# Performance work log

Hardware: AMD Instinct MI355X
Metric: run time of the kernel (lower is better)

## Reference

```python
import jax, jax.numpy as jnp
import numpy as np

EPS = 0.001  # epsilon used by both custom layer norms in the source
B, T, D, H, O = 64, 1024, 128, 256, 64


def setup_inputs() -> dict:
    key = jax.random.key(0)
    ks = jax.random.split(key, 8)
    s = 0.05
    return {
        "x": jax.random.normal(ks[0], (B, T, D), jnp.float32),
        "Wi": jax.random.normal(ks[1], (4 * H, D), jnp.float32) * s,   # input_weights
        "bi": jax.random.normal(ks[2], (4 * H,), jnp.float32) * s,
        "Wh": jax.random.normal(ks[3], (4 * H, H), jnp.float32) * s,   # hidden_weights
        "bh": jax.random.normal(ks[4], (4 * H,), jnp.float32) * s,
        "lna_gamma": jnp.ones((4 * H,), jnp.float32),
        "lna_beta": jnp.zeros((4 * H,), jnp.float32),
        "ln_gamma": jnp.ones((H,), jnp.float32),
        "ln_beta": jnp.zeros((H,), jnp.float32),
        "Wf": jax.random.normal(ks[5], (O, H), jnp.float32) * s,       # fc
        "bf": jax.random.normal(ks[6], (O,), jnp.float32) * s,
    }


def _ln(x, gamma, beta):
    # custom layer norm: mean/var over last axis, eps=1e-3 (no Bessel correction)
    m = jnp.mean(x, axis=-1, keepdims=True)
    xs = x - m
    v = jnp.mean(xs * xs, axis=-1, keepdims=True)
    return gamma * (xs / jnp.sqrt(v + EPS)) + beta


def reference(x, Wi, bi, Wh, bh, lna_gamma, lna_beta, ln_gamma, ln_beta, Wf, bf):
    b, t, d = x.shape
    h = Wh.shape[1]
    # precompute input projections for all timesteps: (T, B, 4H)
    xproj = jnp.einsum('btd,gd->tbg', x, Wi) + bi

    def step(carry, xp_t):
        hx, cx = carry                              # (B, H) each
        gates = xp_t + hx @ Wh.T + bh               # (B, 4H)
        # layer_norm_all: normalize each of the 4 gate blocks over H
        g4 = gates.reshape(b, 4, h)
        m = jnp.mean(g4, axis=-1, keepdims=True)
        gs = g4 - m
        v = jnp.mean(gs * gs, axis=-1, keepdims=True)
        gates = (gs / jnp.sqrt(v + EPS)).reshape(b, 4 * h) * lna_gamma + lna_beta
        ig, fg, cg, og = jnp.split(gates, 4, axis=1)
        ig = jax.nn.sigmoid(ig)
        fg = jax.nn.sigmoid(fg)
        cg = jnp.tanh(cg)
        og = jax.nn.sigmoid(og)
        cy = fg * cx + ig * cg
        hy = og * jnp.tanh(_ln(cy, ln_gamma, ln_beta))
        return (hy, cy), hy

    h0 = jnp.zeros((b, h), x.dtype)
    c0 = jnp.zeros((b, h), x.dtype)
    _, hs = jax.lax.scan(step, (h0, c0), xproj)     # hs: (T, B, H)
    out = hs.transpose(1, 0, 2)                     # (B, T, H)
    yhat = jax.nn.relu(out @ Wf.T + bf)             # (B, T, O)
    return yhat
```

## Files before the change

### kernel.cpp

```cpp
#include <hip/hip_runtime.h>

#define T_TOT 1024
#define BB 64
#define DD 128
#define HH 256
#define GG 1024
#define OO 64
#define LN_EPS 1e-3f
#define NBR 45
#define NBL 19

typedef unsigned int u32;
typedef _Float16 h2 __attribute__((ext_vector_type(2)));
typedef _Float16 f16x8 __attribute__((ext_vector_type(8)));
typedef float f32x4 __attribute__((ext_vector_type(4)));

__device__ __forceinline__ float fdot2(u32 a, u32 b, float c) {
  return __builtin_amdgcn_fdot2(__builtin_bit_cast(h2, a), __builtin_bit_cast(h2, b), c, false);
}
__device__ __forceinline__ u32 pkf16(float lo, float hi) {
  h2 v = { (_Float16)lo, (_Float16)hi };
  return __builtin_bit_cast(u32, v);
}
__device__ __forceinline__ float fast_sigmoid(float x) { return 1.0f / (1.0f + __expf(-x)); }
__device__ __forceinline__ float fast_tanh(float x) { return 2.0f / (1.0f + __expf(-2.0f * x)) - 1.0f; }

__global__ void prep_bfrag(const float* __restrict__ Wh, uint4* __restrict__ bfragG) {
  int id = blockIdx.x * 256 + threadIdx.x;
  int lane = id & 63, tile = (id >> 6) & 63, w = id >> 12;
  int t = tile >> 3, n = tile & 7;
  int col = w * 128 + n * 16 + (lane & 15);
  int k0 = t * 32 + (lane >> 4) * 8;
  const float* p = Wh + (size_t)col * HH + k0;
  uint4 o;
  o.x = pkf16(p[0], p[1]); o.y = pkf16(p[2], p[3]);
  o.z = pkf16(p[4], p[5]); o.w = pkf16(p[6], p[7]);
  bfragG[id] = o;
}

__global__ void prep_wi(const float* __restrict__ Wi, uint4* __restrict__ wip4) {
  int id = blockIdx.x * 256 + threadIdx.x;
  int kp4 = id >> 10, g = id & 1023;
  const float* p = Wi + (size_t)g * DD + kp4 * 8;
  uint4 o;
  o.x = pkf16(p[0], p[1]); o.y = pkf16(p[2], p[3]);
  o.z = pkf16(p[4], p[5]); o.w = pkf16(p[6], p[7]);
  wip4[id] = o;
}

__global__ __launch_bounds__(256) void xproj_gemm(
    const float* __restrict__ x, const uint4* __restrict__ wip4,
    const float* __restrict__ bi, const float* __restrict__ bh,
    _Float16* __restrict__ xph, int m0) {
  __shared__ _Float16 xl[16][128];
  const int tid = threadIdx.x;
  const int mt = blockIdx.x, gt = blockIdx.y;
  const int g = gt * 256 + tid;
  const int woff = ((g >> 7) << 7) | ((g & 15) << 3) | ((g >> 4) & 7);
#pragma unroll
  for (int i = 0; i < 8; ++i) {
    int idx = i * 256 + tid;
    int p = idx >> 7, d = idx & 127;
    int m = m0 + mt * 16 + p;
    xl[p][d] = (_Float16)x[(size_t)(m & 63) * (T_TOT * DD) + (size_t)(m >> 6) * DD + d];
  }
  __syncthreads();
  float acc[16];
#pragma unroll
  for (int p = 0; p < 16; ++p) acc[p] = 0.f;
#pragma unroll
  for (int kp4 = 0; kp4 < 16; ++kp4) {
    uint4 w = wip4[kp4 * GG + g];
#pragma unroll
    for (int p = 0; p < 16; ++p) {
      uint4 hv = *(const uint4*)(&xl[p][kp4 * 8]);
      acc[p] = fdot2(w.x, hv.x, acc[p]);
      acc[p] = fdot2(w.y, hv.y, acc[p]);
      acc[p] = fdot2(w.z, hv.z, acc[p]);
      acc[p] = fdot2(w.w, hv.w, acc[p]);
    }
  }
  float bsum = bi[g] + bh[g];
#pragma unroll
  for (int p = 0; p < 16; ++p) {
    int ml = mt * 16 + p;
    xph[(size_t)ml * GG + woff] = (_Float16)(acc[p] + bsum);
  }
}

__global__ __attribute__((amdgpu_flat_work_group_size(512, 512), amdgpu_waves_per_eu(2, 2)))
void lstm_scan(
    const uint4* __restrict__ bfragG, const _Float16* __restrict__ xphf,
    const float* __restrict__ lna_g, const float* __restrict__ lna_b,
    const float* __restrict__ ln_g, const float* __restrict__ ln_b,
    _Float16* __restrict__ hs16,
    _Float16* __restrict__ hxst, float* __restrict__ cxst,
    int t0, int ct) {
  extern __shared__ char smem[];
  f16x8* wl = (f16x8*)smem;
  _Float16* hx16 = (_Float16*)(smem + 155648);
  float* red  = (float*)(smem + 156160);
  float* red2 = (float*)(smem + 156224);
  float* gact = (float*)(smem + 156256);

  const int tid = threadIdx.x, b = blockIdx.x;
  const int lane = tid & 63, wid = tid >> 6, q = wid >> 1;
  const int l4 = lane & 15;

  const uint4* bw = bfragG + wid * 4096;
  f16x8 breg[NBR];
#pragma unroll
  for (int i = 0; i < NBR; ++i) breg[i] = __builtin_bit_cast(f16x8, bw[i * 64 + lane]);
#pragma unroll
  for (int i = NBR; i < 64; ++i)
    wl[(wid * NBL + (i - NBR)) * 64 + lane] = __builtin_bit_cast(f16x8, bw[i * 64 + lane]);

  u32 lgp[4], lbp[4];
#pragma unroll
  for (int k = 0; k < 4; ++k) {
    int g0 = wid * 128 + (2 * k) * 16 + l4;
    lgp[k] = pkf16(lna_g[g0], lna_g[g0 + 16]);
    lbp[k] = pkf16(lna_b[g0], lna_b[g0 + 16]);
  }
  float lng = 0.f, lnb = 0.f, cx = 0.f;
  if (tid < HH) {
    lng = ln_g[tid]; lnb = ln_b[tid];
    if (t0 == 0) {
      hx16[tid] = (_Float16)0.f;
    } else {
      hx16[tid] = hxst[b * HH + tid]; cx = cxst[b * HH + tid];
    }
  }
  __syncthreads();

  const _Float16* xrow = xphf + (size_t)b * GG + wid * 128 + l4 * 8;
  _Float16* hsp = hs16 + (size_t)b * HH + (tid & 255);

  f16x8 xp = *(const f16x8*)xrow;
  for (int tl = 0; tl < ct; ++tl) {
    f32x4 acc[8];
#pragma unroll
    for (int n = 0; n < 8; ++n) acc[n] = (f32x4){0.f, 0.f, 0.f, 0.f};
#pragma unroll
    for (int t = 0; t < 8; ++t) {
      uint4 hv = *(const uint4*)(hx16 + t * 32 + ((lane >> 4) << 3));
      uint4 az;
      az.x = (l4 == 0) ? hv.x : 0u;
      az.y = (l4 == 0) ? hv.y : 0u;
      az.z = (l4 == 0) ? hv.z : 0u;
      az.w = (l4 == 0) ? hv.w : 0u;
      f16x8 afr = __builtin_bit_cast(f16x8, az);
#pragma unroll
      for (int n = 0; n < 8; ++n) {
        const int idx = t * 8 + n;
        f16x8 bfr;
        if (idx < NBR) bfr = breg[idx];
        else           bfr = wl[(wid * NBL + (idx - NBR)) * 64 + lane];
        acc[n] = __builtin_amdgcn_mfma_f32_16x16x32_f16(afr, bfr, acc[n], 0, 0, 0);
      }
    }
    float g8[8];
#pragma unroll
    for (int n = 0; n < 8; ++n) g8[n] = acc[n][0] + (float)xp[n];
    if (tl + 1 < ct) xp = *(const f16x8*)(xrow + (size_t)(tl + 1) * (BB * GG));

    float s = 0.f, ss = 0.f;
#pragma unroll
    for (int n = 0; n < 8; ++n) { s += g8[n]; ss += g8[n] * g8[n]; }
#pragma unroll
    for (int m = 1; m <= 8; m <<= 1) {
      s += __shfl_xor(s, m, 64);
      ss += __shfl_xor(ss, m, 64);
    }
    if (lane == 0) { red[wid] = s; red[8 + wid] = ss; }
    __syncthreads();
    float S  = red[2 * q] + red[2 * q + 1];
    float SS = red[8 + 2 * q] + red[8 + 2 * q + 1];
    float mean = S * (1.f / HH);
    float var = SS * (1.f / HH) - mean * mean;
    float rstd = rsqrtf(var + LN_EPS);
    if (lane < 16) {
#pragma unroll
      for (int n = 0; n < 8; ++n) {
        h2 lgv = __builtin_bit_cast(h2, lgp[n >> 1]);
        h2 lbv = __builtin_bit_cast(h2, lbp[n >> 1]);
        float gn = (g8[n] - mean) * rstd * (float)lgv[n & 1] + (float)lbv[n & 1];
        float av = (q == 2) ? fast_tanh(gn) : fast_sigmoid(gn);
        gact[wid * 128 + n * 16 + lane] = av;
      }
    }
    __syncthreads();

    float cy = 0.f;
    if (tid < HH) {
      int h = tid;
      cy = gact[HH + h] * cx + gact[h] * gact[2 * HH + h];
      cx = cy;
      float s2 = cy, ss2 = cy * cy;
#pragma unroll
      for (int m = 1; m <= 32; m <<= 1) {
        s2 += __shfl_xor(s2, m, 64);
        ss2 += __shfl_xor(ss2, m, 64);
      }
      if (lane == 0) { red2[wid] = s2; red2[4 + wid] = ss2; }
    }
    __syncthreads();
    if (tid < HH) {
      int h = tid;
      float S2  = red2[0] + red2[1] + red2[2] + red2[3];
      float SS2 = red2[4] + red2[5] + red2[6] + red2[7];
      float mc = S2 * (1.f / HH);
      float vc = SS2 * (1.f / HH) - mc * mc;
      float cyn = (cy - mc) * rsqrtf(vc + LN_EPS) * lng + lnb;
      float hy = gact[3 * HH + h] * fast_tanh(cyn);
      hx16[h] = (_Float16)hy;
      hsp[(size_t)(t0 + tl) * (BB * HH)] = (_Float16)hy;
    }
    __syncthreads();
  }
  if (tid < HH) { hxst[b * HH + tid] = hx16[tid]; cxst[b * HH + tid] = cx; }
}

__global__ __launch_bounds__(256) void out_gemm(
    const _Float16* __restrict__ hs16, const float* __restrict__ Wf,
    const float* __restrict__ bf, float* __restrict__ out) {
  __shared__ u32 wfl[128][64];
  __shared__ u32 hsl[16][132];
  const int tid = threadIdx.x;
  const int mbase = blockIdx.x * 16;
#pragma unroll
  for (int i = 0; i < 32; ++i) {
    int idx = i * 256 + tid;
    int kp = idx >> 6, o = idx & 63;
    wfl[kp][o] = pkf16(Wf[o * HH + kp * 2], Wf[o * HH + kp * 2 + 1]);
  }
#pragma unroll
  for (int i = 0; i < 8; ++i) {
    int idx = i * 256 + tid;
    int p = idx >> 7, kp = idx & 127;
    hsl[p][kp] = *(const u32*)(hs16 + (size_t)(mbase + p) * HH + kp * 2);
  }
  __syncthreads();
  const int o = tid & 63, mi = tid >> 6;
  float bfo = bf[o];
#pragma unroll
  for (int mm = mi; mm < 16; mm += 4) {
    float a0 = bfo, a1 = 0.f, a2 = 0.f, a3 = 0.f;
#pragma unroll
    for (int kp = 0; kp < 128; kp += 4) {
      a0 = fdot2(wfl[kp + 0][o], hsl[mm][kp + 0], a0);
      a1 = fdot2(wfl[kp + 1][o], hsl[mm][kp + 1], a1);
      a2 = fdot2(wfl[kp + 2][o], hsl[mm][kp + 2], a2);
      a3 = fdot2(wfl[kp + 3][o], hsl[mm][kp + 3], a3);
    }
    float r = (a0 + a1) + (a2 + a3);
    int m = mbase + mm;
    out[(size_t)(m & 63) * (T_TOT * OO) + (size_t)(m >> 6) * OO + o] = fmaxf(r, 0.f);
  }
}

extern "C" void kernel_launch(void* const* d_in, const int* in_sizes, int n_in,
                              void* d_out, int out_size, void* d_ws, size_t ws_size,
                              hipStream_t stream) {
  if (n_in < 11) return;
  const float* x    = (const float*)d_in[0];
  const float* Wi   = (const float*)d_in[1];
  const float* bi   = (const float*)d_in[2];
  const float* Wh   = (const float*)d_in[3];
  const float* bh   = (const float*)d_in[4];
  const float* lnag = (const float*)d_in[5];
  const float* lnab = (const float*)d_in[6];
  const float* lng  = (const float*)d_in[7];
  const float* lnb  = (const float*)d_in[8];
  const float* Wf   = (const float*)d_in[9];
  const float* bf   = (const float*)d_in[10];
  float* out = (float*)d_out;

  char* ws = (char*)d_ws;
  uint4* bfragG = (uint4*)ws;
  uint4* wip4 = (uint4*)(ws + (512 << 10));
  _Float16* hs16 = (_Float16*)(ws + (1 << 20));
  _Float16* hxst = (_Float16*)(ws + (1 << 20) + (32 << 20));
  float* cxst = (float*)(ws + (1 << 20) + (32 << 20) + (64 << 10));
  const size_t xph_off = (size_t)35 << 20;
  _Float16* xph = (_Float16*)(ws + xph_off);

  size_t avail = ws_size > xph_off ? ws_size - xph_off : 0;
  int ct = T_TOT;
  while (ct > 1 && (size_t)ct * (BB * GG * 2) > avail) ct >>= 1;

  const int scan_smem = 160352;
  (void)hipFuncSetAttribute(reinterpret_cast<const void*>(lstm_scan),
                            hipFuncAttributeMaxDynamicSharedMemorySize, scan_smem);

  prep_bfrag<<<128, 256, 0, stream>>>(Wh, bfragG);
  prep_wi<<<64, 256, 0, stream>>>(Wi, wip4);
  for (int t0 = 0; t0 < T_TOT; t0 += ct) {
    xproj_gemm<<<dim3((ct * BB) / 16, 4), 256, 0, stream>>>(x, wip4, bi, bh, xph, t0 * BB);
    lstm_scan<<<BB, 512, scan_smem, stream>>>(bfragG, xph, lnag, lnab, lng, lnb,
                                              hs16, hxst, cxst, t0, ct);
  }
  out_gemm<<<(T_TOT * BB) / 16, 256, 0, stream>>>(hs16, Wf, bf, out);
}
```

Measured before the change: 3.610 ms.

## Stream most Wh fragments from global/L2 with double-buffered registers instead of keeping them resident

Instead of holding 45 weight fragments per wave in registers and the remaining 19 in LDS, each wave now keeps 16 fragments in static LDS and reloads the other 48 from global memory on every timestep. The reloads go through two 8-fragment register buffers that are double-buffered and issued ahead of the MFMAs that use them. This lowers register pressure and drops the large dynamic LDS allocation. In exchange it adds a large amount of global/L2 traffic on the serial recurrence critical path every step, and load latency may not be fully hidden.

```diff
diff --git a/kernel.cpp b/kernel.cpp
--- a/kernel.cpp
+++ b/kernel.cpp
@@ -7,8 +7,8 @@
 #define GG 1024
 #define OO 64
 #define LN_EPS 1e-3f
-#define NBR 45
-#define NBL 19
+#define NLT 16
+#define NST 48
 
 typedef unsigned int u32;
 typedef _Float16 h2 __attribute__((ext_vector_type(2)));
@@ -24,6 +24,13 @@
 }
 __device__ __forceinline__ float fast_sigmoid(float x) { return 1.0f / (1.0f + __expf(-x)); }
 __device__ __forceinline__ float fast_tanh(float x) { return 2.0f / (1.0f + __expf(-2.0f * x)) - 1.0f; }
+
+#define AFRAG(t) \
+    uint4 hv = *(const uint4*)(hx16 + (t) * 32 + ((lane >> 4) << 3)); \
+    uint4 az; \
+    az.x = (l4 == 0) ? hv.x : 0u; az.y = (l4 == 0) ? hv.y : 0u; \
+    az.z = (l4 == 0) ? hv.z : 0u; az.w = (l4 == 0) ? hv.w : 0u; \
+    f16x8 afr = __builtin_bit_cast(f16x8, az);
 
 __global__ void prep_bfrag(const float* __restrict__ Wh, uint4* __restrict__ bfragG) {
   int id = blockIdx.x * 256 + threadIdx.x;
@@ -88,32 +95,28 @@
   }
 }
 
-__global__ __attribute__((amdgpu_flat_work_group_size(512, 512), amdgpu_waves_per_eu(2, 2)))
-void lstm_scan(
+__global__ __launch_bounds__(512) void lstm_scan(
     const uint4* __restrict__ bfragG, const _Float16* __restrict__ xphf,
     const float* __restrict__ lna_g, const float* __restrict__ lna_b,
     const float* __restrict__ ln_g, const float* __restrict__ ln_b,
     _Float16* __restrict__ hs16,
     _Float16* __restrict__ hxst, float* __restrict__ cxst,
     int t0, int ct) {
-  extern __shared__ char smem[];
-  f16x8* wl = (f16x8*)smem;
-  _Float16* hx16 = (_Float16*)(smem + 155648);
-  float* red  = (float*)(smem + 156160);
-  float* red2 = (float*)(smem + 156224);
-  float* gact = (float*)(smem + 156256);
+  __shared__ uint4 wl[8 * NLT * 64];
+  __shared__ _Float16 hx16[HH];
+  __shared__ float red[16];
+  __shared__ float red2[8];
+  __shared__ float gact[GG];
 
   const int tid = threadIdx.x, b = blockIdx.x;
   const int lane = tid & 63, wid = tid >> 6, q = wid >> 1;
   const int l4 = lane & 15;
 
   const uint4* bw = bfragG + wid * 4096;
-  f16x8 breg[NBR];
-#pragma unroll
-  for (int i = 0; i < NBR; ++i) breg[i] = __builtin_bit_cast(f16x8, bw[i * 64 + lane]);
-#pragma unroll
-  for (int i = NBR; i < 64; ++i)
-    wl[(wid * NBL + (i - NBR)) * 64 + lane] = __builtin_bit_cast(f16x8, bw[i * 64 + lane]);
+#pragma unroll
+  for (int i = 0; i < NLT; ++i)
+    wl[(wid * NLT + i) * 64 + lane] = bw[i * 64 + lane];
+  const uint4* stream = bw + NLT * 64;
 
   u32 lgp[4], lbp[4];
 #pragma unroll
@@ -125,11 +128,8 @@
   float lng = 0.f, lnb = 0.f, cx = 0.f;
   if (tid < HH) {
     lng = ln_g[tid]; lnb = ln_b[tid];
-    if (t0 == 0) {
-      hx16[tid] = (_Float16)0.f;
-    } else {
-      hx16[tid] = hxst[b * HH + tid]; cx = cxst[b * HH + tid];
-    }
+    if (t0 == 0) hx16[tid] = (_Float16)0.f;
+    else { hx16[tid] = hxst[b * HH + tid]; cx = cxst[b * HH + tid]; }
   }
   __syncthreads();
 
@@ -138,27 +138,70 @@
 
   f16x8 xp = *(const f16x8*)xrow;
   for (int tl = 0; tl < ct; ++tl) {
+    uint4 s0[8], s1[8];
+#pragma unroll
+    for (int i = 0; i < 8; ++i) s0[i] = stream[(0 * 8 + i) * 64 + lane];
+#pragma unroll
+    for (int i = 0; i < 8; ++i) s1[i] = stream[(1 * 8 + i) * 64 + lane];
+
     f32x4 acc[8];
 #pragma unroll
     for (int n = 0; n < 8; ++n) acc[n] = (f32x4){0.f, 0.f, 0.f, 0.f};
-#pragma unroll
-    for (int t = 0; t < 8; ++t) {
-      uint4 hv = *(const uint4*)(hx16 + t * 32 + ((lane >> 4) << 3));
-      uint4 az;
-      az.x = (l4 == 0) ? hv.x : 0u;
-      az.y = (l4 == 0) ? hv.y : 0u;
-      az.z = (l4 == 0) ? hv.z : 0u;
-      az.w = (l4 == 0) ? hv.w : 0u;
-      f16x8 afr = __builtin_bit_cast(f16x8, az);
+
+#pragma unroll
+    for (int t = 0; t < 2; ++t) {
+      AFRAG(t);
 #pragma unroll
       for (int n = 0; n < 8; ++n) {
-        const int idx = t * 8 + n;
-        f16x8 bfr;
-        if (idx < NBR) bfr = breg[idx];
-        else           bfr = wl[(wid * NBL + (idx - NBR)) * 64 + lane];
+        f16x8 bfr = __builtin_bit_cast(f16x8, wl[(wid * NLT + t * 8 + n) * 64 + lane]);
         acc[n] = __builtin_amdgcn_mfma_f32_16x16x32_f16(afr, bfr, acc[n], 0, 0, 0);
       }
     }
+    {
+      AFRAG(2);
+#pragma unroll
+      for (int n = 0; n < 8; ++n)
+        acc[n] = __builtin_amdgcn_mfma_f32_16x16x32_f16(afr, __builtin_bit_cast(f16x8, s0[n]), acc[n], 0, 0, 0);
+#pragma unroll
+      for (int i = 0; i < 8; ++i) s0[i] = stream[(2 * 8 + i) * 64 + lane];
+    }
+    {
+      AFRAG(3);
+#pragma unroll
+      for (int n = 0; n < 8; ++n)
+        acc[n] = __builtin_amdgcn_mfma_f32_16x16x32_f16(afr, __builtin_bit_cast(f16x8, s1[n]), acc[n], 0, 0, 0);
+#pragma unroll
+      for (int i = 0; i < 8; ++i) s1[i] = stream[(3 * 8 + i) * 64 + lane];
+    }
+    {
+      AFRAG(4);
+#pragma unroll
+      for (int n = 0; n < 8; ++n)
+        acc[n] = __builtin_amdgcn_mfma_f32_16x16x32_f16(afr, __builtin_bit_cast(f16x8, s0[n]), acc[n], 0, 0, 0);
+#pragma unroll
+      for (int i = 0; i < 8; ++i) s0[i] = stream[(4 * 8 + i) * 64 + lane];
+    }
+    {
+      AFRAG(5);
+#pragma unroll
+      for (int n = 0; n < 8; ++n)
+        acc[n] = __builtin_amdgcn_mfma_f32_16x16x32_f16(afr, __builtin_bit_cast(f16x8, s1[n]), acc[n], 0, 0, 0);
+#pragma unroll
+      for (int i = 0; i < 8; ++i) s1[i] = stream[(5 * 8 + i) * 64 + lane];
+    }
+    {
+      AFRAG(6);
+#pragma unroll
+      for (int n = 0; n < 8; ++n)
+        acc[n] = __builtin_amdgcn_mfma_f32_16x16x32_f16(afr, __builtin_bit_cast(f16x8, s0[n]), acc[n], 0, 0, 0);
+    }
+    {
+      AFRAG(7);
+#pragma unroll
+      for (int n = 0; n < 8; ++n)
+        acc[n] = __builtin_amdgcn_mfma_f32_16x16x32_f16(afr, __builtin_bit_cast(f16x8, s1[n]), acc[n], 0, 0, 0);
+    }
+
     float g8[8];
 #pragma unroll
     for (int n = 0; n < 8; ++n) g8[n] = acc[n][0] + (float)xp[n];
@@ -289,16 +332,12 @@
   int ct = T_TOT;
   while (ct > 1 && (size_t)ct * (BB * GG * 2) > avail) ct >>= 1;
 
-  const int scan_smem = 160352;
-  (void)hipFuncSetAttribute(reinterpret_cast<const void*>(lstm_scan),
-                            hipFuncAttributeMaxDynamicSharedMemorySize, scan_smem);
-
   prep_bfrag<<<128, 256, 0, stream>>>(Wh, bfragG);
   prep_wi<<<64, 256, 0, stream>>>(Wi, wip4);
   for (int t0 = 0; t0 < T_TOT; t0 += ct) {
     xproj_gemm<<<dim3((ct * BB) / 16, 4), 256, 0, stream>>>(x, wip4, bi, bh, xph, t0 * BB);
-    lstm_scan<<<BB, 512, scan_smem, stream>>>(bfragG, xph, lnag, lnab, lng, lnb,
-                                              hs16, hxst, cxst, t0, ct);
+    lstm_scan<<<BB, 512, 0, stream>>>(bfragG, xph, lnag, lnab, lng, lnb,
+                                      hs16, hxst, cxst, t0, ct);
   }
   out_gemm<<<(T_TOT * BB) / 16, 256, 0, stream>>>(hs16, Wf, bf, out);
 }
```

After: 4.804 ms. +33.1%, slower.
